# Kernel tuning notes

Measured on AMD Instinct MI355X. Metric: run time of the kernel, lower is better.

## Reference

```python
import jax, jax.numpy as jnp
import numpy as np

N, E, EMB, HID, FT, H = 2000, 32000, 768, 384, 768, 4
NEG_SLOPE = 0.2


def gat_conv(x, src, dst, edge_attr, W, a_src, a_dst, W_e, a_e, b):
    """PyG GATConv, concat=False (mean over heads), edge_dim, add_self_loops
    with fill_value='mean'. x:[N,Fin], edge_attr:[E,768]."""
    n = x.shape[0]
    h, c = a_src.shape
    # self loops: edge_attr of loop (i,i) = mean of incoming edge_attr at i
    deg = jax.ops.segment_sum(jnp.ones(src.shape[0], x.dtype), dst, num_segments=n)
    loop_attr = jax.ops.segment_sum(edge_attr, dst, num_segments=n) / jnp.maximum(deg, 1.0)[:, None]
    ar = jnp.arange(n)
    s = jnp.concatenate([src, ar])
    d = jnp.concatenate([dst, ar])
    ea = jnp.concatenate([edge_attr, loop_attr], axis=0)   # [E+N, 768]
    hx = (x @ W).reshape(n, h, c)                           # [N,H,C]
    he = (ea @ W_e).reshape(-1, h, c)                       # [E+N,H,C]
    alpha = (jnp.einsum('nhc,hc->nh', hx, a_src)[s]
             + jnp.einsum('nhc,hc->nh', hx, a_dst)[d]
             + jnp.einsum('ehc,hc->eh', he, a_e))           # [E+N,H]
    alpha = jax.nn.leaky_relu(alpha, NEG_SLOPE)
    # segment softmax over destination node (self loop guarantees nonempty)
    mx = jax.ops.segment_max(alpha, d, num_segments=n)
    ex = jnp.exp(alpha - mx[d])
    den = jax.ops.segment_sum(ex, d, num_segments=n)
    att = ex / den[d]                                       # [E+N,H]
    out = jax.ops.segment_sum(hx[s] * att[:, :, None], d, num_segments=n)  # [N,H,C]
    return out.mean(axis=1) + b


def setup_inputs() -> dict:
    key = jax.random.key(0)
    ks = jax.random.split(key, 16)
    w = lambda k, shape, s=0.05: (jax.random.normal(k, shape, jnp.float32) * s)
    return {
        'x': jax.random.randint(ks[0], (N, 2), 0, 178),
        'edge_index': jax.random.randint(ks[1], (2, E), 0, N),
        'edge_attr': jax.random.randint(ks[2], (E, 2), 0, 18),
        'x_emb': w(ks[3], (178, EMB)),
        'e_emb': w(ks[4], (18, EMB)),
        'W1': w(ks[5], (EMB, H * HID)),
        'as1': w(ks[6], (H, HID)),
        'ad1': w(ks[7], (H, HID)),
        'We1': w(ks[8], (EMB, H * HID)),
        'ae1': w(ks[9], (H, HID)),
        'b1': jnp.zeros((HID,), jnp.float32),
        'W2': w(ks[10], (HID, H * FT)),
        'as2': w(ks[11], (H, FT)),
        'ad2': w(ks[12], (H, FT)),
        'We2': w(ks[13], (EMB, H * FT)),
        'ae2': w(ks[14], (H, FT)),
        'b2': jnp.zeros((FT,), jnp.float32),
    }


def reference(x, edge_index, edge_attr, x_emb, e_emb, W1, as1, ad1, We1, ae1, b1,
              W2, as2, ad2, We2, ae2, b2):
    src, dst = edge_index[0], edge_index[1]
    xf = x_emb[x].sum(axis=1)          # [N,768]
    eaf = e_emb[edge_attr].sum(axis=1)  # [E,768]
    h = jax.nn.relu(gat_conv(xf, src, dst, eaf, W1, as1, ad1, We1, ae1, b1))
    out = gat_conv(h, src, dst, eaf, W2, as2, ad2, We2, ae2, b2)
    return out
```

## Files before the change

kernel.cpp:

```cpp
#include <hip/hip_runtime.h>
#include <hip/hip_bf16.h>

#define NN   2000
#define NE   32000
#define EMBD 768
#define NH   4
#define HID  384
#define FTD  768
#define NEG  0.2f
#define DCAP 128

#define GM 2000
#define GN 768
#define GK 1536

typedef __bf16 bf16x8 __attribute__((ext_vector_type(8)));
typedef float  f32x4  __attribute__((ext_vector_type(4)));

__device__ inline float wsum(float v){
#pragma unroll
  for (int o = 32; o > 0; o >>= 1) v += __shfl_xor(v, o, 64);
  return v;
}
__device__ inline float wmax(float v){
#pragma unroll
  for (int o = 32; o > 0; o >>= 1) v = fmaxf(v, __shfl_xor(v, o, 64));
  return v;
}

__device__ inline unsigned short f2bf(float f){
  unsigned u = __float_as_uint(f);
  unsigned r = (u + 0x7FFFu + ((u >> 16) & 1u)) >> 16;
  return (unsigned short)r;
}
__device__ inline float bf2f(unsigned short h){
  return __uint_as_float(((unsigned)h) << 16);
}

__device__ inline void gload16(const void* g, void* l){
  __builtin_amdgcn_global_load_lds((const __attribute__((address_space(1))) void*)g,
                                   (__attribute__((address_space(3))) void*)l, 16, 0, 0);
}

__global__ void k_zero(int* __restrict__ counts){
  int i = blockIdx.x * blockDim.x + threadIdx.x;
  if (i < NN) counts[i] = 0;
}

__global__ void k_count(const int* __restrict__ dst, int* __restrict__ counts){
  int e = blockIdx.x * blockDim.x + threadIdx.x;
  if (e < NE) atomicAdd(&counts[dst[e]], 1);
}

__global__ void k_scan(const int* __restrict__ counts, int* __restrict__ offsets,
                       int* __restrict__ cursor){
  __shared__ int s[1024];
  int t = threadIdx.x;
  int a = (2*t   < NN) ? counts[2*t  ] : 0;
  int b = (2*t+1 < NN) ? counts[2*t+1] : 0;
  s[t] = a + b;
  __syncthreads();
  for (int off = 1; off < 1024; off <<= 1){
    int v = (t >= off) ? s[t-off] : 0;
    __syncthreads();
    s[t] += v;
    __syncthreads();
  }
  int base = (t > 0) ? s[t-1] : 0;
  if (2*t < NN){ offsets[2*t] = base; cursor[2*t] = base; }
  if (2*t+1 < NN){ offsets[2*t+1] = base + a; cursor[2*t+1] = base + a; }
  if (2*t == NN) offsets[NN] = base;
}

__global__ void k_fill(const int* __restrict__ dst, int* __restrict__ cursor,
                       int* __restrict__ csr){
  int e = blockIdx.x * blockDim.x + threadIdx.x;
  if (e < NE){
    int p = atomicAdd(&cursor[dst[e]], 1);
    csr[p] = e;
  }
}

__global__ __launch_bounds__(256) void k_prep1(
    const float* __restrict__ We1, const float* __restrict__ ae1,
    const float* __restrict__ W2,  const float* __restrict__ as2,
    const float* __restrict__ ad2, const float* __restrict__ We2,
    const float* __restrict__ ae2,
    float* __restrict__ we_a1, float* __restrict__ wa_s2,
    float* __restrict__ wa_d2, float* __restrict__ we_a2){
  int wid = blockIdx.x*4 + (threadIdx.x >> 6);
  int lane = threadIdx.x & 63;
  if (wid < 3072){
    int k = wid >> 2, h = wid & 3;
    const float4* wr = (const float4*)(We1 + (size_t)k*1536 + h*384);
    const float4* ap = (const float4*)(ae1 + h*384);
    float4 w0 = wr[lane], a0 = ap[lane];
    float s = w0.x*a0.x + w0.y*a0.y + w0.z*a0.z + w0.w*a0.w;
    if (lane < 32){
      float4 w1 = wr[64+lane], a1 = ap[64+lane];
      s += w1.x*a1.x + w1.y*a1.y + w1.z*a1.z + w1.w*a1.w;
    }
    s = wsum(s);
    if (lane == 0) we_a1[k*4+h] = s;
  } else if (wid < 4608){
    int t2 = wid - 3072;
    int k = t2 >> 2, h = t2 & 3;
    const float4* wr = (const float4*)(W2 + (size_t)k*3072 + h*768);
    const float4* s4 = (const float4*)(as2 + h*768);
    const float4* d4 = (const float4*)(ad2 + h*768);
    float s1 = 0.f, s2 = 0.f;
#pragma unroll
    for (int i = 0; i < 3; ++i){
      float4 w = wr[i*64+lane], a = s4[i*64+lane], d = d4[i*64+lane];
      s1 += w.x*a.x + w.y*a.y + w.z*a.z + w.w*a.w;
      s2 += w.x*d.x + w.y*d.y + w.z*d.z + w.w*d.w;
    }
    s1 = wsum(s1); s2 = wsum(s2);
    if (lane == 0){ wa_s2[k*4+h] = s1; wa_d2[k*4+h] = s2; }
  } else {
    int t2 = wid - 4608;
    int k = t2 >> 2, h = t2 & 3;
    const float4* wr = (const float4*)(We2 + (size_t)k*3072 + h*768);
    const float4* ap = (const float4*)(ae2 + h*768);
    float s = 0.f;
#pragma unroll
    for (int i = 0; i < 3; ++i){
      float4 w = wr[i*64+lane], a = ap[i*64+lane];
      s += w.x*a.x + w.y*a.y + w.z*a.z + w.w*a.w;
    }
    s = wsum(s);
    if (lane == 0) we_a2[k*4+h] = s;
  }
}

__global__ __launch_bounds__(256) void k_bt(const float* __restrict__ W2,
                                            unsigned short* __restrict__ Bh,
                                            unsigned short* __restrict__ Bl){
  __shared__ float tile[64][65];
  int bk = blockIdx.x * 64;
  int bc = blockIdx.y * 64;
  int t = threadIdx.x;
  int cc = t & 63, kk4 = t >> 6;
#pragma unroll
  for (int i = 0; i < 16; ++i){
    int kk = kk4*16 + i;
    int k = bk + kk;
    int h = k / 384, kp = k - h*384;
    tile[kk][cc] = W2[(size_t)kp*3072 + h*768 + bc + cc];
  }
  __syncthreads();
  int kk2 = t & 63, cc4 = t >> 6;
#pragma unroll
  for (int i = 0; i < 16; ++i){
    int c2 = cc4*16 + i;
    float v = tile[kk2][c2];
    unsigned short hi = f2bf(v);
    unsigned short lo = f2bf(v - bf2f(hi));
    size_t o = (size_t)(bc + c2)*GK + bk + kk2;
    Bh[o] = hi; Bl[o] = lo;
  }
}

__global__ __launch_bounds__(256) void k_gemm1(const float* __restrict__ A,
                                               const float* __restrict__ B,
                                               float* __restrict__ P){
  __shared__ float As[16][34];
  __shared__ float Bs[16][68];
  int t = threadIdx.x;
  int bn = blockIdx.x * 64;
  int bm = blockIdx.y * 32;
  int s  = blockIdx.z;
  float acc[2][4] = {};
  int tm = t >> 4, tn = t & 15;
  int ar = t >> 3, ac = (t & 7) * 2;
  int br = t >> 4, bc = (t & 15) * 4;
  int kend = s*384 + 384;
  for (int k0 = s*384; k0 < kend; k0 += 16){
    float a0 = 0.f, a1 = 0.f;
    if (bm + ar < 178){
      const float* ap = &A[(size_t)(bm+ar)*EMBD + k0 + ac];
      a0 = ap[0]; a1 = ap[1];
    }
    As[ac][ar] = a0; As[ac+1][ar] = a1;
    *(float4*)&Bs[br][bc] = *(const float4*)&B[(size_t)(k0+br)*1536 + bn + bc];
    __syncthreads();
#pragma unroll
    for (int k = 0; k < 16; ++k){
      float x0 = As[k][tm*2], x1 = As[k][tm*2+1];
      float4 b4 = *(const float4*)&Bs[k][tn*4];
      acc[0][0] += x0*b4.x; acc[0][1] += x0*b4.y; acc[0][2] += x0*b4.z; acc[0][3] += x0*b4.w;
      acc[1][0] += x1*b4.x; acc[1][1] += x1*b4.y; acc[1][2] += x1*b4.z; acc[1][3] += x1*b4.w;
    }
    __syncthreads();
  }
#pragma unroll
  for (int i = 0; i < 2; ++i){
    int r = bm + tm*2 + i;
    if (r < 178){
      float4 v; v.x=acc[i][0]; v.y=acc[i][1]; v.z=acc[i][2]; v.w=acc[i][3];
      *(float4*)&P[(size_t)s*178*1536 + (size_t)r*1536 + bn + tn*4] = v;
    }
  }
}

__global__ __launch_bounds__(256) void k_prepB(
    const float* __restrict__ parts, float* __restrict__ xh1,
    const float* __restrict__ as1, const float* __restrict__ ad1,
    const float* __restrict__ e_emb,
    const float* __restrict__ we_a1, const float* __restrict__ we_a2,
    float* __restrict__ xa_s1, float* __restrict__ xa_d1,
    float* __restrict__ ew1, float* __restrict__ ew2){
  int blk = blockIdx.x, t = threadIdx.x;
  if (blk < 267){
    int i = blk*256 + t;
    float4 u = ((const float4*)parts)[i];
    float4 v = ((const float4*)parts)[68352 + i];
    float4 r; r.x=u.x+v.x; r.y=u.y+v.y; r.z=u.z+v.z; r.w=u.w+v.w;
    ((float4*)xh1)[i] = r;
  } else if (blk < 445){
    int r = blk - 267;
    int h = t >> 6, lane = t & 63;
    const float4* p0 = (const float4*)(parts + (size_t)r*1536 + h*384);
    const float4* p1 = (const float4*)(parts + (size_t)(178 + r)*1536 + h*384);
    const float4* s4 = (const float4*)(as1 + h*384);
    const float4* d4 = (const float4*)(ad1 + h*384);
    float s1, s2;
    {
      float4 a = p0[lane], b = p1[lane], sa = s4[lane], da = d4[lane];
      float4 u; u.x=a.x+b.x; u.y=a.y+b.y; u.z=a.z+b.z; u.w=a.w+b.w;
      s1 = u.x*sa.x + u.y*sa.y + u.z*sa.z + u.w*sa.w;
      s2 = u.x*da.x + u.y*da.y + u.z*da.z + u.w*da.w;
    }
    if (lane < 32){
      float4 a = p0[64+lane], b = p1[64+lane], sa = s4[64+lane], da = d4[64+lane];
      float4 u; u.x=a.x+b.x; u.y=a.y+b.y; u.z=a.z+b.z; u.w=a.w+b.w;
      s1 += u.x*sa.x + u.y*sa.y + u.z*sa.z + u.w*sa.w;
      s2 += u.x*da.x + u.y*da.y + u.z*da.z + u.w*da.w;
    }
    s1 = wsum(s1); s2 = wsum(s2);
    if (lane == 0){ xa_s1[r*4+h] = s1; xa_d1[r*4+h] = s2; }
  } else {
    int id = (blk - 445)*4 + (t >> 6);
    int lane = t & 63;
    const float* wv = (id < 72) ? we_a1 : we_a2;
    float* o = (id < 72) ? ew1 : ew2;
    int id2 = (id < 72) ? id : (id - 72);
    int r = id2 >> 2, h = id2 & 3;
    const float* ar = e_emb + (size_t)r*EMBD;
    float acc = 0.f;
    for (int k = lane; k < EMBD; k += 64) acc += ar[k] * wv[k*4+h];
    acc = wsum(acc);
    if (lane == 0) o[r*4+h] = acc;
  }
}

__global__ __launch_bounds__(384) void k_gat1(const int* __restrict__ offsets,
                      int* __restrict__ csr, const int* __restrict__ srcv,
                      const int* __restrict__ x, const int* __restrict__ ea,
                      const float* __restrict__ xa_s1, const float* __restrict__ xa_d1,
                      const float* __restrict__ ew1,
                      const float* __restrict__ xh1, const float* __restrict__ b1,
                      const float* __restrict__ wa_s2, const float* __restrict__ wa_d2,
                      float* __restrict__ spill,
                      float* __restrict__ hact,
                      float* __restrict__ asrc2, float* __restrict__ adst2){
  __shared__ float wts[DCAP][5];
  __shared__ int   sE[DCAP];
  __shared__ int   sA[DCAP], sB[DCAP];
  __shared__ float wl[4];
  __shared__ float red[6][8];
  int n = blockIdx.x, t = threadIdx.x;
  int w = t >> 6, lane = t & 63;
  int lo = offsets[n], hi = offsets[n+1];
  int deg = hi - lo;
  bool big = deg > DCAP;

  if (!big){
    int m = 1; while (m < deg) m <<= 1;
    for (int i = t; i < m; i += 384) sE[i] = (i < deg) ? csr[lo+i] : 0x7fffffff;
    __syncthreads();
    for (int k = 2; k <= m; k <<= 1){
      for (int j2 = k >> 1; j2 > 0; j2 >>= 1){
        for (int i = t; i < m; i += 384){
          int ixj = i ^ j2;
          if (ixj > i){
            int a = sE[i], b = sE[ixj];
            bool up = ((i & k) == 0);
            if ((a > b) == up){ sE[i] = b; sE[ixj] = a; }
          }
        }
        __syncthreads();
      }
    }
    for (int i = t; i < deg; i += 384) csr[lo+i] = sE[i];
  } else {
    if (t == 0){
      for (int i = lo+1; i < hi; ++i){
        int v = csr[i], j = i-1;
        while (j >= lo && csr[j] > v){ csr[j+1] = csr[j]; --j; }
        csr[j+1] = v;
      }
    }
  }
  __syncthreads();

  int xn0 = x[2*n], xn1 = x[2*n+1];
  if (w < 4){
    float ad_n = xa_d1[xn0*4+w] + xa_d1[xn1*4+w];
    float as_n = xa_s1[xn0*4+w] + xa_s1[xn1*4+w];
    float mx = -3.4e38f, sae = 0.f;
    if (!big){
      for (int j = lane; j < deg; j += 64){
        int e = sE[j]; int s = srcv[e];
        int a = x[2*s], b = x[2*s+1];
        if (w == 0){ sA[j] = a; sB[j] = b; }
        float ae = ew1[ea[2*e]*4+w] + ew1[ea[2*e+1]*4+w];
        float al = (xa_s1[a*4+w] + xa_s1[b*4+w]) + ad_n + ae;
        al = (al > 0.f) ? al : NEG * al;
        wts[j][w] = al;
        sae += ae; mx = fmaxf(mx, al);
      }
      mx = wmax(mx); sae = wsum(sae);
      float all_ = as_n + ad_n + sae / fmaxf((float)deg, 1.f);
      all_ = (all_ > 0.f) ? all_ : NEG * all_;
      mx = fmaxf(mx, all_);
      float den = 0.f;
      for (int j = lane; j < deg; j += 64){
        float xx = expf(wts[j][w] - mx);
        wts[j][w] = xx; den += xx;
      }
      den = wsum(den);
      float exl = expf(all_ - mx);
      den += exl;
      float inv = 1.f / den;
      for (int j = lane; j < deg; j += 64) wts[j][w] *= inv;
      if (lane == 0) wl[w] = exl * inv;
    } else {
      for (int p = lo + lane; p < hi; p += 64){
        int e = csr[p]; int s = srcv[e];
        int a = x[2*s], b = x[2*s+1];
        float ae = ew1[ea[2*e]*4+w] + ew1[ea[2*e+1]*4+w];
        float al = (xa_s1[a*4+w] + xa_s1[b*4+w]) + ad_n + ae;
        al = (al > 0.f) ? al : NEG * al;
        spill[e*4 + w] = al;
        sae += ae; mx = fmaxf(mx, al);
      }
      mx = wmax(mx); sae = wsum(sae);
      float all_ = as_n + ad_n + sae / fmaxf((float)deg, 1.f);
      all_ = (all_ > 0.f) ? all_ : NEG * all_;
      mx = fmaxf(mx, all_);
      float den = 0.f;
      for (int p = lo + lane; p < hi; p += 64){
        int e = csr[p];
        float xx = expf(spill[e*4 + w] - mx);
        spill[e*4 + w] = xx; den += xx;
      }
      den = wsum(den);
      float exl = expf(all_ - mx);
      den += exl;
      float inv = 1.f / den;
      for (int p = lo + lane; p < hi; p += 64) spill[csr[p]*4 + w] *= inv;
      if (lane == 0) wl[w] = exl * inv;
    }
  }
  __syncthreads();

  int c = t;
  float acc = 0.f;
  if (!big){
    float va0=0,va1=0,va2=0,va3=0,vb0=0,vb1=0,vb2=0,vb3=0;
    if (deg > 0){
      const float* pa = xh1 + (size_t)sA[0]*1536 + c;
      const float* pb = xh1 + (size_t)sB[0]*1536 + c;
      va0=pa[0]; va1=pa[384]; va2=pa[768]; va3=pa[1152];
      vb0=pb[0]; vb1=pb[384]; vb2=pb[768]; vb3=pb[1152];
    }
    for (int j = 0; j < deg; ++j){
      float ca0=va0, ca1=va1, ca2=va2, ca3=va3;
      float cb0=vb0, cb1=vb1, cb2=vb2, cb3=vb3;
      if (j+1 < deg){
        const float* pa = xh1 + (size_t)sA[j+1]*1536 + c;
        const float* pb = xh1 + (size_t)sB[j+1]*1536 + c;
        va0=pa[0]; va1=pa[384]; va2=pa[768]; va3=pa[1152];
        vb0=pb[0]; vb1=pb[384]; vb2=pb[768]; vb3=pb[1152];
      }
      float w0=wts[j][0], w1=wts[j][1], w2=wts[j][2], w3=wts[j][3];
      acc += w0*(ca0+cb0) + w1*(ca1+cb1) + w2*(ca2+cb2) + w3*(ca3+cb3);
    }
  } else {
    for (int j = 0; j < deg; ++j){
      int e = csr[lo+j]; int s = srcv[e];
      int a = x[2*s], b = x[2*s+1];
      float w0 = spill[e*4+0], w1 = spill[e*4+1], w2 = spill[e*4+2], w3 = spill[e*4+3];
      const float* pa = xh1 + (size_t)a*1536 + c;
      const float* pb = xh1 + (size_t)b*1536 + c;
      acc += w0*(pa[0]+pb[0]) + w1*(pa[384]+pb[384])
           + w2*(pa[768]+pb[768]) + w3*(pa[1152]+pb[1152]);
    }
  }
  {
    const float* pa = xh1 + (size_t)xn0*1536 + c;
    const float* pb = xh1 + (size_t)xn1*1536 + c;
    acc += wl[0]*(pa[0]+pb[0]) + wl[1]*(pa[384]+pb[384])
         + wl[2]*(pa[768]+pb[768]) + wl[3]*(pa[1152]+pb[1152]);
  }
  float v = fmaxf(0.25f*acc + b1[c], 0.f);
  hact[n*HID + c] = v;

  float pr[8];
#pragma unroll
  for (int h = 0; h < 4; ++h){ pr[h] = v * wa_s2[c*4+h]; pr[4+h] = v * wa_d2[c*4+h]; }
#pragma unroll
  for (int o = 32; o > 0; o >>= 1){
#pragma unroll
    for (int q = 0; q < 8; ++q) pr[q] += __shfl_xor(pr[q], o, 64);
  }
  if (lane == 0){
#pragma unroll
    for (int q = 0; q < 8; ++q) red[w][q] = pr[q];
  }
  __syncthreads();
  if (t < 8){
    float s2 = 0.f;
#pragma unroll
    for (int ww = 0; ww < 6; ++ww) s2 += red[ww][t];
    if (t < 4) asrc2[n*4 + t] = s2; else adst2[n*4 + t - 4] = s2;
  }
}

__global__ __launch_bounds__(384) void k_gat2(const int* __restrict__ offsets,
                      const int* __restrict__ csr, const int* __restrict__ srcv,
                      const int* __restrict__ ea,
                      const float* __restrict__ asrc, const float* __restrict__ adst,
                      const float* __restrict__ ew2,
                      const float* __restrict__ hact, float* __restrict__ spill,
                      unsigned short* __restrict__ Gh, unsigned short* __restrict__ Gl){
  __shared__ float wts[DCAP][5];
  __shared__ int   ssrc[DCAP];
  __shared__ float wl[4];
  int n = blockIdx.x, t = threadIdx.x;
  int w = t >> 6, lane = t & 63;
  int lo = offsets[n], hi = offsets[n+1];
  int deg = hi - lo;
  bool big = deg > DCAP;
  if (w < 4){
    float ad_n = adst[n*NH + w];
    float as_n = asrc[n*NH + w];
    float mx = -3.4e38f, sae = 0.f;
    if (!big){
      for (int p = lo + lane; p < hi; p += 64){
        int e = csr[p]; int s = srcv[e];
        if (w == 0) ssrc[p - lo] = s;
        float ae = ew2[ea[2*e]*4+w] + ew2[ea[2*e+1]*4+w];
        float al = asrc[s*NH + w] + ad_n + ae;
        al = (al > 0.f) ? al : NEG * al;
        wts[p - lo][w] = al;
        sae += ae; mx = fmaxf(mx, al);
      }
      mx = wmax(mx); sae = wsum(sae);
      float all_ = as_n + ad_n + sae / fmaxf((float)deg, 1.f);
      all_ = (all_ > 0.f) ? all_ : NEG * all_;
      mx = fmaxf(mx, all_);
      float den = 0.f;
      for (int p = lo + lane; p < hi; p += 64){
        float xx = expf(wts[p - lo][w] - mx);
        wts[p - lo][w] = xx; den += xx;
      }
      den = wsum(den);
      float exl = expf(all_ - mx);
      den += exl;
      float inv = 1.f / den;
      for (int p = lo + lane; p < hi; p += 64) wts[p - lo][w] *= inv;
      if (lane == 0) wl[w] = exl * inv;
    } else {
      for (int p = lo + lane; p < hi; p += 64){
        int e = csr[p];
        float ae = ew2[ea[2*e]*4+w] + ew2[ea[2*e+1]*4+w];
        float al = asrc[srcv[e]*NH + w] + ad_n + ae;
        al = (al > 0.f) ? al : NEG * al;
        spill[e*4 + w] = al;
        sae += ae; mx = fmaxf(mx, al);
      }
      mx = wmax(mx); sae = wsum(sae);
      float all_ = as_n + ad_n + sae / fmaxf((float)deg, 1.f);
      all_ = (all_ > 0.f) ? all_ : NEG * all_;
      mx = fmaxf(mx, all_);
      float den = 0.f;
      for (int p = lo + lane; p < hi; p += 64){
        int e = csr[p];
        float xx = expf(spill[e*4 + w] - mx);
        spill[e*4 + w] = xx; den += xx;
      }
      den = wsum(den);
      float exl = expf(all_ - mx);
      den += exl;
      float inv = 1.f / den;
      for (int p = lo + lane; p < hi; p += 64) spill[csr[p]*4 + w] *= inv;
      if (lane == 0) wl[w] = exl * inv;
    }
  }
  __syncthreads();

  int c = t;
  float a0 = 0.f, a1 = 0.f, a2 = 0.f, a3 = 0.f;
  if (!big){
    float vnext = 0.f;
    if (deg > 0) vnext = hact[(size_t)ssrc[0]*HID + c];
    for (int j = 0; j < deg; ++j){
      float vc = vnext;
      if (j+1 < deg) vnext = hact[(size_t)ssrc[j+1]*HID + c];
      float w0=wts[j][0], w1=wts[j][1], w2=wts[j][2], w3=wts[j][3];
      a0 += w0*vc; a1 += w1*vc; a2 += w2*vc; a3 += w3*vc;
    }
  } else {
    for (int j = 0; j < deg; ++j){
      int e = csr[lo+j]; int s = srcv[e];
      float w0 = spill[e*4+0], w1 = spill[e*4+1], w2 = spill[e*4+2], w3 = spill[e*4+3];
      float vc = hact[(size_t)s*HID + c];
      a0 += w0*vc; a1 += w1*vc; a2 += w2*vc; a3 += w3*vc;
    }
  }
  {
    float vc = hact[(size_t)n*HID + c];
    a0 += wl[0]*vc; a1 += wl[1]*vc; a2 += wl[2]*vc; a3 += wl[3]*vc;
  }
  size_t base = (size_t)n*GK + c;
  float vv[4] = {a0, a1, a2, a3};
#pragma unroll
  for (int h = 0; h < 4; ++h){
    unsigned short hi16 = f2bf(vv[h]);
    unsigned short lo16 = f2bf(vv[h] - bf2f(hi16));
    Gh[base + h*384] = hi16;
    Gl[base + h*384] = lo16;
  }
}

__global__ __launch_bounds__(256) void k_mm2(const unsigned short* __restrict__ Gh,
                                             const unsigned short* __restrict__ Gl,
                                             const unsigned short* __restrict__ Bh,
                                             const unsigned short* __restrict__ Bl,
                                             const float* __restrict__ b2,
                                             float* __restrict__ out){
  __shared__ __align__(16) unsigned short lds[2][4][64][64];
  int b = blockIdx.x;
  int xcd = b & 7, idx = b >> 3;
  int bm = xcd*4 + idx/12, bn = idx % 12;
  int wave = threadIdx.x >> 6, lane = threadIdx.x & 63;
  int wm = wave >> 1, wn = wave & 1;
  int rl = lane & 15, kq = lane >> 4;

  int rt   = lane >> 3;
  int kswz = ((lane & 7) ^ rt) * 8;
  const unsigned short* sbase;
  int rowbase;
  if (wave == 0){ sbase = Gh; rowbase = bm*64; }
  else if (wave == 1){ sbase = Gl; rowbase = bm*64; }
  else if (wave == 2){ sbase = Bh; rowbase = bn*64; }
  else { sbase = Bl; rowbase = bn*64; }
  bool isA = wave < 2;

  f32x4 acc[2][2] = {};

#pragma unroll
  for (int i = 0; i < 8; ++i){
    int row = rowbase + i*8 + rt;
    if (isA) row = (row < GM) ? row : (GM-1);
    gload16(sbase + (size_t)row*GK + kswz, &lds[0][wave][i*8][0]);
  }
  __syncthreads();

  for (int t = 0; t < 24; ++t){
    int cur = t & 1;
    if (t < 23){
      int k0 = (t+1)*64;
#pragma unroll
      for (int i = 0; i < 8; ++i){
        int row = rowbase + i*8 + rt;
        if (isA) row = (row < GM) ? row : (GM-1);
        gload16(sbase + (size_t)row*GK + k0 + kswz, &lds[cur^1][wave][i*8][0]);
      }
    }
#pragma unroll
    for (int ks = 0; ks < 2; ++ks){
      bf16x8 ah[2], al2[2], bh2[2], bl2[2];
#pragma unroll
      for (int i = 0; i < 2; ++i){
        int r = wm*32 + i*16 + rl;
        int sl = (ks*4 + kq) ^ (r & 7);
        ah[i]  = *(const bf16x8*)&lds[cur][0][r][sl*8];
        al2[i] = *(const bf16x8*)&lds[cur][1][r][sl*8];
      }
#pragma unroll
      for (int j = 0; j < 2; ++j){
        int cdx = wn*32 + j*16 + rl;
        int sl = (ks*4 + kq) ^ (cdx & 7);
        bh2[j] = *(const bf16x8*)&lds[cur][2][cdx][sl*8];
        bl2[j] = *(const bf16x8*)&lds[cur][3][cdx][sl*8];
      }
#pragma unroll
      for (int i = 0; i < 2; ++i){
#pragma unroll
        for (int j = 0; j < 2; ++j){
          acc[i][j] = __builtin_amdgcn_mfma_f32_16x16x32_bf16(ah[i],  bh2[j], acc[i][j], 0, 0, 0);
          acc[i][j] = __builtin_amdgcn_mfma_f32_16x16x32_bf16(ah[i],  bl2[j], acc[i][j], 0, 0, 0);
          acc[i][j] = __builtin_amdgcn_mfma_f32_16x16x32_bf16(al2[i], bh2[j], acc[i][j], 0, 0, 0);
        }
      }
    }
    __syncthreads();
  }

#pragma unroll
  for (int i = 0; i < 2; ++i){
#pragma unroll
    for (int j = 0; j < 2; ++j){
      int col = bn*64 + wn*32 + j*16 + rl;
      float bb = b2[col];
#pragma unroll
      for (int r = 0; r < 4; ++r){
        int row = bm*64 + wm*32 + i*16 + kq*4 + r;
        if (row < GM) out[(size_t)row*GN + col] = 0.25f*acc[i][j][r] + bb;
      }
    }
  }
}

extern "C" void kernel_launch(void* const* d_in, const int* in_sizes, int n_in,
                              void* d_out, int out_size, void* d_ws, size_t ws_size,
                              hipStream_t stream){
  const int*   x     = (const int*)d_in[0];
  const int*   ei    = (const int*)d_in[1];
  const int*   ea    = (const int*)d_in[2];
  const float* x_emb = (const float*)d_in[3];
  const float* e_emb = (const float*)d_in[4];
  const float* W1    = (const float*)d_in[5];
  const float* as1   = (const float*)d_in[6];
  const float* ad1   = (const float*)d_in[7];
  const float* We1   = (const float*)d_in[8];
  const float* ae1   = (const float*)d_in[9];
  const float* b1    = (const float*)d_in[10];
  const float* W2    = (const float*)d_in[11];
  const float* as2   = (const float*)d_in[12];
  const float* ad2   = (const float*)d_in[13];
  const float* We2   = (const float*)d_in[14];
  const float* ae2   = (const float*)d_in[15];
  const float* b2    = (const float*)d_in[16];
  const int* srcv = ei;
  const int* dstv = ei + NE;
  float* out = (float*)d_out;

  char* p = (char*)d_ws;
  auto take = [&](size_t n){ void* q = (void*)p; p += (n + 255) & ~(size_t)255; return q; };
  int*   counts  = (int*)take(NN*4);
  int*   cursor  = (int*)take(NN*4);
  int*   offsets = (int*)take((NN+1)*4);
  int*   csr     = (int*)take(NE*4);
  float* we_a1   = (float*)take(EMBD*NH*4);
  float* wa_s2   = (float*)take(HID*NH*4);
  float* wa_d2   = (float*)take(HID*NH*4);
  float* we_a2   = (float*)take(EMBD*NH*4);
  float* xa_s1   = (float*)take(178*NH*4);
  float* xa_d1   = (float*)take(178*NH*4);
  float* ew1     = (float*)take(18*NH*4);
  float* ew2     = (float*)take(18*NH*4);
  float* xh1     = (float*)take((size_t)178*1536*4);
  float* parts1  = (float*)take((size_t)2*178*1536*4);
  unsigned short* Bth = (unsigned short*)take((size_t)GN*GK*2);
  unsigned short* Btl = (unsigned short*)take((size_t)GN*GK*2);
  unsigned short* Gh  = (unsigned short*)take((size_t)GM*GK*2);
  unsigned short* Gl  = (unsigned short*)take((size_t)GM*GK*2);
  float* spill   = (float*)take((size_t)NE*NH*4);
  float* hact    = (float*)take((size_t)NN*HID*4);
  float* asrc2   = (float*)take(NN*NH*4);
  float* adst2   = (float*)take(NN*NH*4);

  k_zero<<<8, 256, 0, stream>>>(counts);
  k_count<<<(NE+255)/256, 256, 0, stream>>>(dstv, counts);
  k_scan<<<1, 1024, 0, stream>>>(counts, offsets, cursor);
  k_fill<<<(NE+255)/256, 256, 0, stream>>>(dstv, cursor, csr);

  k_prep1<<<1920, 256, 0, stream>>>(We1, ae1, W2, as2, ad2, We2, ae2,
                                    we_a1, wa_s2, wa_d2, we_a2);
  { dim3 g(GK/64, GN/64); k_bt<<<g, 256, 0, stream>>>(W2, Bth, Btl); }
  { dim3 g(24, 6, 2); k_gemm1<<<g, 256, 0, stream>>>(x_emb, W1, parts1); }
  k_prepB<<<481, 256, 0, stream>>>(parts1, xh1, as1, ad1, e_emb, we_a1, we_a2,
                                   xa_s1, xa_d1, ew1, ew2);

  k_gat1<<<NN, 384, 0, stream>>>(offsets, csr, srcv, x, ea, xa_s1, xa_d1, ew1,
                                 xh1, b1, wa_s2, wa_d2, spill, hact, asrc2, adst2);

  k_gat2<<<NN, 384, 0, stream>>>(offsets, csr, srcv, ea, asrc2, adst2, ew2,
                                 hact, spill, Gh, Gl);

  k_mm2<<<384, 256, 0, stream>>>(Gh, Gl, Bth, Btl, b2, out);
}
```

Baseline: 132.0 us.

## Reformulate layer-1 aggregation as per-token coefficient matrix times bf16x3 MFMA GEMM

Layer-1 aggregation is rewritten to exploit the fact that node features come from only 178 embedding tokens. Each node accumulates attention weights per (head, token) into a 768-wide coefficient row, split into bf16 hi/lo parts. A new MFMA GEMM then multiplies this matrix by a transposed, padded per-token projection table to produce the hidden activations. This replaces per-edge gathers of 1536-float rows with a dense GEMM; the attention-score dot products move into a separate small kernel. The serial lane-0 scatter into shared memory and the extra launches add cost in exchange.

```diff
diff --git a/kernel.cpp b/kernel.cpp
--- a/kernel.cpp
+++ b/kernel.cpp
@@ -6,13 +6,13 @@
 #define EMBD 768
 #define NH   4
 #define HID  384
-#define FTD  768
 #define NEG  0.2f
 #define DCAP 128
 
 #define GM 2000
 #define GN 768
 #define GK 1536
+#define K1 768
 
 typedef __bf16 bf16x8 __attribute__((ext_vector_type(8)));
 typedef float  f32x4  __attribute__((ext_vector_type(4)));
@@ -204,21 +204,25 @@
 }
 
 __global__ __launch_bounds__(256) void k_prepB(
-    const float* __restrict__ parts, float* __restrict__ xh1,
+    const float* __restrict__ parts,
     const float* __restrict__ as1, const float* __restrict__ ad1,
     const float* __restrict__ e_emb,
     const float* __restrict__ we_a1, const float* __restrict__ we_a2,
+    unsigned short* __restrict__ XHh, unsigned short* __restrict__ XHl,
     float* __restrict__ xa_s1, float* __restrict__ xa_d1,
     float* __restrict__ ew1, float* __restrict__ ew2){
   int blk = blockIdx.x, t = threadIdx.x;
-  if (blk < 267){
-    int i = blk*256 + t;
-    float4 u = ((const float4*)parts)[i];
-    float4 v = ((const float4*)parts)[68352 + i];
-    float4 r; r.x=u.x+v.x; r.y=u.y+v.y; r.z=u.z+v.z; r.w=u.w+v.w;
-    ((float4*)xh1)[i] = r;
-  } else if (blk < 445){
-    int r = blk - 267;
+  if (blk < 178){
+    int tok = blk;
+    for (int i = t; i < 1536; i += 256){
+      float v = parts[(size_t)tok*1536 + i] + parts[(size_t)(178+tok)*1536 + i];
+      int h = i / 384, c = i - h*384;
+      size_t off = (size_t)c*K1 + h*192 + tok;
+      unsigned short hi = f2bf(v);
+      XHh[off] = hi; XHl[off] = f2bf(v - bf2f(hi));
+    }
+  } else if (blk < 356){
+    int r = blk - 178;
     int h = t >> 6, lane = t & 63;
     const float4* p0 = (const float4*)(parts + (size_t)r*1536 + h*384);
     const float4* p1 = (const float4*)(parts + (size_t)(178 + r)*1536 + h*384);
@@ -239,8 +243,8 @@
     }
     s1 = wsum(s1); s2 = wsum(s2);
     if (lane == 0){ xa_s1[r*4+h] = s1; xa_d1[r*4+h] = s2; }
-  } else {
-    int id = (blk - 445)*4 + (t >> 6);
+  } else if (blk < 392){
+    int id = (blk - 356)*4 + (t >> 6);
     int lane = t & 63;
     const float* wv = (id < 72) ? we_a1 : we_a2;
     float* o = (id < 72) ? ew1 : ew2;
@@ -251,24 +255,27 @@
     for (int k = lane; k < EMBD; k += 64) acc += ar[k] * wv[k*4+h];
     acc = wsum(acc);
     if (lane == 0) o[r*4+h] = acc;
-  }
-}
-
-__global__ __launch_bounds__(384) void k_gat1(const int* __restrict__ offsets,
+  } else {
+    int i = (blk - 392)*256 + t;
+    if (i < 21504){
+      int c = i / 56, rem = i - c*56;
+      int h = rem / 14, tp = 178 + rem - h*14;
+      size_t off = (size_t)c*K1 + h*192 + tp;
+      XHh[off] = 0; XHl[off] = 0;
+    }
+  }
+}
+
+__global__ __launch_bounds__(256) void k_gat1sm(const int* __restrict__ offsets,
                       int* __restrict__ csr, const int* __restrict__ srcv,
                       const int* __restrict__ x, const int* __restrict__ ea,
                       const float* __restrict__ xa_s1, const float* __restrict__ xa_d1,
-                      const float* __restrict__ ew1,
-                      const float* __restrict__ xh1, const float* __restrict__ b1,
-                      const float* __restrict__ wa_s2, const float* __restrict__ wa_d2,
-                      float* __restrict__ spill,
-                      float* __restrict__ hact,
-                      float* __restrict__ asrc2, float* __restrict__ adst2){
+                      const float* __restrict__ ew1, float* __restrict__ spill,
+                      unsigned short* __restrict__ Qh, unsigned short* __restrict__ Ql){
   __shared__ float wts[DCAP][5];
   __shared__ int   sE[DCAP];
   __shared__ int   sA[DCAP], sB[DCAP];
-  __shared__ float wl[4];
-  __shared__ float red[6][8];
+  __shared__ float coef[K1];
   int n = blockIdx.x, t = threadIdx.x;
   int w = t >> 6, lane = t & 63;
   int lo = offsets[n], hi = offsets[n+1];
@@ -277,11 +284,11 @@
 
   if (!big){
     int m = 1; while (m < deg) m <<= 1;
-    for (int i = t; i < m; i += 384) sE[i] = (i < deg) ? csr[lo+i] : 0x7fffffff;
+    for (int i = t; i < m; i += 256) sE[i] = (i < deg) ? csr[lo+i] : 0x7fffffff;
     __syncthreads();
     for (int k = 2; k <= m; k <<= 1){
       for (int j2 = k >> 1; j2 > 0; j2 >>= 1){
-        for (int i = t; i < m; i += 384){
+        for (int i = t; i < m; i += 256){
           int ixj = i ^ j2;
           if (ixj > i){
             int a = sE[i], b = sE[ixj];
@@ -292,7 +299,7 @@
         __syncthreads();
       }
     }
-    for (int i = t; i < deg; i += 384) csr[lo+i] = sE[i];
+    for (int i = t; i < deg; i += 256) csr[lo+i] = sE[i];
   } else {
     if (t == 0){
       for (int i = lo+1; i < hi; ++i){
@@ -302,114 +309,201 @@
       }
     }
   }
+  for (int i = t; i < K1; i += 256) coef[i] = 0.f;
   __syncthreads();
 
   int xn0 = x[2*n], xn1 = x[2*n+1];
-  if (w < 4){
-    float ad_n = xa_d1[xn0*4+w] + xa_d1[xn1*4+w];
-    float as_n = xa_s1[xn0*4+w] + xa_s1[xn1*4+w];
-    float mx = -3.4e38f, sae = 0.f;
+  float ad_n = xa_d1[xn0*4+w] + xa_d1[xn1*4+w];
+  float as_n = xa_s1[xn0*4+w] + xa_s1[xn1*4+w];
+  float mx = -3.4e38f, sae = 0.f;
+  float wlv;
+  if (!big){
+    for (int j = lane; j < deg; j += 64){
+      int e = sE[j]; int s = srcv[e];
+      int a = x[2*s], b = x[2*s+1];
+      if (w == 0){ sA[j] = a; sB[j] = b; }
+      float ae = ew1[ea[2*e]*4+w] + ew1[ea[2*e+1]*4+w];
+      float al = (xa_s1[a*4+w] + xa_s1[b*4+w]) + ad_n + ae;
+      al = (al > 0.f) ? al : NEG * al;
+      wts[j][w] = al;
+      sae += ae; mx = fmaxf(mx, al);
+    }
+    mx = wmax(mx); sae = wsum(sae);
+    float all_ = as_n + ad_n + sae / fmaxf((float)deg, 1.f);
+    all_ = (all_ > 0.f) ? all_ : NEG * all_;
+    mx = fmaxf(mx, all_);
+    float den = 0.f;
+    for (int j = lane; j < deg; j += 64){
+      float xx = expf(wts[j][w] - mx);
+      wts[j][w] = xx; den += xx;
+    }
+    den = wsum(den);
+    float exl = expf(all_ - mx);
+    den += exl;
+    float inv = 1.f / den;
+    for (int j = lane; j < deg; j += 64) wts[j][w] *= inv;
+    wlv = exl * inv;
+  } else {
+    for (int p = lo + lane; p < hi; p += 64){
+      int e = csr[p]; int s = srcv[e];
+      int a = x[2*s], b = x[2*s+1];
+      float ae = ew1[ea[2*e]*4+w] + ew1[ea[2*e+1]*4+w];
+      float al = (xa_s1[a*4+w] + xa_s1[b*4+w]) + ad_n + ae;
+      al = (al > 0.f) ? al : NEG * al;
+      spill[e*4 + w] = al;
+      sae += ae; mx = fmaxf(mx, al);
+    }
+    mx = wmax(mx); sae = wsum(sae);
+    float all_ = as_n + ad_n + sae / fmaxf((float)deg, 1.f);
+    all_ = (all_ > 0.f) ? all_ : NEG * all_;
+    mx = fmaxf(mx, all_);
+    float den = 0.f;
+    for (int p = lo + lane; p < hi; p += 64){
+      int e = csr[p];
+      float xx = expf(spill[e*4 + w] - mx);
+      spill[e*4 + w] = xx; den += xx;
+    }
+    den = wsum(den);
+    float exl = expf(all_ - mx);
+    den += exl;
+    float inv = 1.f / den;
+    for (int p = lo + lane; p < hi; p += 64) spill[csr[p]*4 + w] *= inv;
+    wlv = exl * inv;
+  }
+  __syncthreads();
+
+  if (lane == 0){
+    float* cf = coef + w*192;
     if (!big){
-      for (int j = lane; j < deg; j += 64){
-        int e = sE[j]; int s = srcv[e];
-        int a = x[2*s], b = x[2*s+1];
-        if (w == 0){ sA[j] = a; sB[j] = b; }
-        float ae = ew1[ea[2*e]*4+w] + ew1[ea[2*e+1]*4+w];
-        float al = (xa_s1[a*4+w] + xa_s1[b*4+w]) + ad_n + ae;
-        al = (al > 0.f) ? al : NEG * al;
-        wts[j][w] = al;
-        sae += ae; mx = fmaxf(mx, al);
-      }
-      mx = wmax(mx); sae = wsum(sae);
-      float all_ = as_n + ad_n + sae / fmaxf((float)deg, 1.f);
-      all_ = (all_ > 0.f) ? all_ : NEG * all_;
-      mx = fmaxf(mx, all_);
-      float den = 0.f;
-      for (int j = lane; j < deg; j += 64){
-        float xx = expf(wts[j][w] - mx);
-        wts[j][w] = xx; den += xx;
-      }
-      den = wsum(den);
-      float exl = expf(all_ - mx);
-      den += exl;
-      float inv = 1.f / den;
-      for (int j = lane; j < deg; j += 64) wts[j][w] *= inv;
-      if (lane == 0) wl[w] = exl * inv;
+      for (int j = 0; j < deg; ++j){
+        float wj = wts[j][w];
+        cf[sA[j]] += wj; cf[sB[j]] += wj;
+      }
     } else {
-      for (int p = lo + lane; p < hi; p += 64){
+      for (int p = lo; p < hi; ++p){
         int e = csr[p]; int s = srcv[e];
-        int a = x[2*s], b = x[2*s+1];
-        float ae = ew1[ea[2*e]*4+w] + ew1[ea[2*e+1]*4+w];
-        float al = (xa_s1[a*4+w] + xa_s1[b*4+w]) + ad_n + ae;
-        al = (al > 0.f) ? al : NEG * al;
-        spill[e*4 + w] = al;
-        sae += ae; mx = fmaxf(mx, al);
-      }
-      mx = wmax(mx); sae = wsum(sae);
-      float all_ = as_n + ad_n + sae / fmaxf((float)deg, 1.f);
-      all_ = (all_ > 0.f) ? all_ : NEG * all_;
-      mx = fmaxf(mx, all_);
-      float den = 0.f;
-      for (int p = lo + lane; p < hi; p += 64){
-        int e = csr[p];
-        float xx = expf(spill[e*4 + w] - mx);
-        spill[e*4 + w] = xx; den += xx;
-      }
-      den = wsum(den);
-      float exl = expf(all_ - mx);
-      den += exl;
-      float inv = 1.f / den;
-      for (int p = lo + lane; p < hi; p += 64) spill[csr[p]*4 + w] *= inv;
-      if (lane == 0) wl[w] = exl * inv;
-    }
+        float wj = spill[e*4 + w];
+        cf[x[2*s]] += wj; cf[x[2*s+1]] += wj;
+      }
+    }
+    cf[xn0] += wlv; cf[xn1] += wlv;
   }
   __syncthreads();
 
-  int c = t;
-  float acc = 0.f;
-  if (!big){
-    float va0=0,va1=0,va2=0,va3=0,vb0=0,vb1=0,vb2=0,vb3=0;
-    if (deg > 0){
-      const float* pa = xh1 + (size_t)sA[0]*1536 + c;
-      const float* pb = xh1 + (size_t)sB[0]*1536 + c;
-      va0=pa[0]; va1=pa[384]; va2=pa[768]; va3=pa[1152];
-      vb0=pb[0]; vb1=pb[384]; vb2=pb[768]; vb3=pb[1152];
-    }
-    for (int j = 0; j < deg; ++j){
-      float ca0=va0, ca1=va1, ca2=va2, ca3=va3;
-      float cb0=vb0, cb1=vb1, cb2=vb2, cb3=vb3;
-      if (j+1 < deg){
-        const float* pa = xh1 + (size_t)sA[j+1]*1536 + c;
-        const float* pb = xh1 + (size_t)sB[j+1]*1536 + c;
-        va0=pa[0]; va1=pa[384]; va2=pa[768]; va3=pa[1152];
-        vb0=pb[0]; vb1=pb[384]; vb2=pb[768]; vb3=pb[1152];
-      }
-      float w0=wts[j][0], w1=wts[j][1], w2=wts[j][2], w3=wts[j][3];
-      acc += w0*(ca0+cb0) + w1*(ca1+cb1) + w2*(ca2+cb2) + w3*(ca3+cb3);
-    }
-  } else {
-    for (int j = 0; j < deg; ++j){
-      int e = csr[lo+j]; int s = srcv[e];
-      int a = x[2*s], b = x[2*s+1];
-      float w0 = spill[e*4+0], w1 = spill[e*4+1], w2 = spill[e*4+2], w3 = spill[e*4+3];
-      const float* pa = xh1 + (size_t)a*1536 + c;
-      const float* pb = xh1 + (size_t)b*1536 + c;
-      acc += w0*(pa[0]+pb[0]) + w1*(pa[384]+pb[384])
-           + w2*(pa[768]+pb[768]) + w3*(pa[1152]+pb[1152]);
-    }
-  }
-  {
-    const float* pa = xh1 + (size_t)xn0*1536 + c;
-    const float* pb = xh1 + (size_t)xn1*1536 + c;
-    acc += wl[0]*(pa[0]+pb[0]) + wl[1]*(pa[384]+pb[384])
-         + wl[2]*(pa[768]+pb[768]) + wl[3]*(pa[1152]+pb[1152]);
-  }
-  float v = fmaxf(0.25f*acc + b1[c], 0.f);
-  hact[n*HID + c] = v;
-
-  float pr[8];
-#pragma unroll
-  for (int h = 0; h < 4; ++h){ pr[h] = v * wa_s2[c*4+h]; pr[4+h] = v * wa_d2[c*4+h]; }
+  for (int i = t; i < K1; i += 256){
+    float v = coef[i];
+    unsigned short hi16 = f2bf(v);
+    Qh[(size_t)n*K1 + i] = hi16;
+    Ql[(size_t)n*K1 + i] = f2bf(v - bf2f(hi16));
+  }
+}
+
+__global__ __launch_bounds__(256) void k_mm1(const unsigned short* __restrict__ Qh,
+                                             const unsigned short* __restrict__ Ql,
+                                             const unsigned short* __restrict__ XHh,
+                                             const unsigned short* __restrict__ XHl,
+                                             const float* __restrict__ b1,
+                                             float* __restrict__ hact){
+  __shared__ __align__(16) unsigned short lds[2][4][64][64];
+  int b = blockIdx.x;
+  int xcd = b & 7, idx = b >> 3;
+  int bm = xcd*4 + idx/6, bn = idx % 6;
+  int wave = threadIdx.x >> 6, lane = threadIdx.x & 63;
+  int wm = wave >> 1, wn = wave & 1;
+  int rl = lane & 15, kq = lane >> 4;
+
+  int rt   = lane >> 3;
+  int kswz = ((lane & 7) ^ rt) * 8;
+  const unsigned short* sbase;
+  int rowbase;
+  if (wave == 0){ sbase = Qh; rowbase = bm*64; }
+  else if (wave == 1){ sbase = Ql; rowbase = bm*64; }
+  else if (wave == 2){ sbase = XHh; rowbase = bn*64; }
+  else { sbase = XHl; rowbase = bn*64; }
+  bool isA = wave < 2;
+
+  f32x4 acc[2][2] = {};
+
+#pragma unroll
+  for (int i = 0; i < 8; ++i){
+    int row = rowbase + i*8 + rt;
+    if (isA) row = (row < GM) ? row : (GM-1);
+    gload16(sbase + (size_t)row*K1 + kswz, &lds[0][wave][i*8][0]);
+  }
+  __syncthreads();
+
+  for (int t = 0; t < 12; ++t){
+    int cur = t & 1;
+    if (t < 11){
+      int k0 = (t+1)*64;
+#pragma unroll
+      for (int i = 0; i < 8; ++i){
+        int row = rowbase + i*8 + rt;
+        if (isA) row = (row < GM) ? row : (GM-1);
+        gload16(sbase + (size_t)row*K1 + k0 + kswz, &lds[cur^1][wave][i*8][0]);
+      }
+    }
+#pragma unroll
+    for (int ks = 0; ks < 2; ++ks){
+      bf16x8 ah[2], al2[2], bh2[2], bl2[2];
+#pragma unroll
+      for (int i = 0; i < 2; ++i){
+        int r = wm*32 + i*16 + rl;
+        int sl = (ks*4 + kq) ^ (r & 7);
+        ah[i]  = *(const bf16x8*)&lds[cur][0][r][sl*8];
+        al2[i] = *(const bf16x8*)&lds[cur][1][r][sl*8];
+      }
+#pragma unroll
+      for (int j = 0; j < 2; ++j){
+        int cdx = wn*32 + j*16 + rl;
+        int sl = (ks*4 + kq) ^ (cdx & 7);
+        bh2[j] = *(const bf16x8*)&lds[cur][2][cdx][sl*8];
+        bl2[j] = *(const bf16x8*)&lds[cur][3][cdx][sl*8];
+      }
+#pragma unroll
+      for (int i = 0; i < 2; ++i){
+#pragma unroll
+        for (int j = 0; j < 2; ++j){
+          acc[i][j] = __builtin_amdgcn_mfma_f32_16x16x32_bf16(ah[i],  bh2[j], acc[i][j], 0, 0, 0);
+          acc[i][j] = __builtin_amdgcn_mfma_f32_16x16x32_bf16(ah[i],  bl2[j], acc[i][j], 0, 0, 0);
+          acc[i][j] = __builtin_amdgcn_mfma_f32_16x16x32_bf16(al2[i], bh2[j], acc[i][j], 0, 0, 0);
+        }
+      }
+    }
+    __syncthreads();
+  }
+
+#pragma unroll
+  for (int i = 0; i < 2; ++i){
+#pragma unroll
+    for (int j = 0; j < 2; ++j){
+      int col = bn*64 + wn*32 + j*16 + rl;
+      float bb = b1[col];
+#pragma unroll
+      for (int r = 0; r < 4; ++r){
+        int row = bm*64 + wm*32 + i*16 + kq*4 + r;
+        if (row < GM) hact[(size_t)row*HID + col] = fmaxf(0.25f*acc[i][j][r] + bb, 0.f);
+      }
+    }
+  }
+}
+
+__global__ __launch_bounds__(256) void k_dots(const float* __restrict__ hact,
+                      const float* __restrict__ wa_s2, const float* __restrict__ wa_d2,
+                      float* __restrict__ asrc2, float* __restrict__ adst2){
+  int w = threadIdx.x >> 6, lane = threadIdx.x & 63;
+  int n = blockIdx.x*4 + w;
+  float pr[8] = {};
+#pragma unroll
+  for (int i = 0; i < 6; ++i){
+    int c = i*64 + lane;
+    float v = hact[(size_t)n*HID + c];
+#pragma unroll
+    for (int h = 0; h < 4; ++h){
+      pr[h]   += v * wa_s2[c*4+h];
+      pr[4+h] += v * wa_d2[c*4+h];
+    }
+  }
 #pragma unroll
   for (int o = 32; o > 0; o >>= 1){
 #pragma unroll
@@ -417,14 +511,7 @@
   }
   if (lane == 0){
 #pragma unroll
-    for (int q = 0; q < 8; ++q) red[w][q] = pr[q];
-  }
-  __syncthreads();
-  if (t < 8){
-    float s2 = 0.f;
-#pragma unroll
-    for (int ww = 0; ww < 6; ++ww) s2 += red[ww][t];
-    if (t < 4) asrc2[n*4 + t] = s2; else adst2[n*4 + t - 4] = s2;
+    for (int h = 0; h < 4; ++h){ asrc2[n*4+h] = pr[h]; adst2[n*4+h] = pr[4+h]; }
   }
 }
 
@@ -663,8 +750,11 @@
   float* xa_d1   = (float*)take(178*NH*4);
   float* ew1     = (float*)take(18*NH*4);
   float* ew2     = (float*)take(18*NH*4);
-  float* xh1     = (float*)take((size_t)178*1536*4);
   float* parts1  = (float*)take((size_t)2*178*1536*4);
+  unsigned short* XHh = (unsigned short*)take((size_t)HID*K1*2);
+  unsigned short* XHl = (unsigned short*)take((size_t)HID*K1*2);
+  unsigned short* Qh  = (unsigned short*)take((size_t)NN*K1*2);
+  unsigned short* Ql  = (unsigned short*)take((size_t)NN*K1*2);
   unsigned short* Bth = (unsigned short*)take((size_t)GN*GK*2);
   unsigned short* Btl = (unsigned short*)take((size_t)GN*GK*2);
   unsigned short* Gh  = (unsigned short*)take((size_t)GM*GK*2);
@@ -683,11 +773,13 @@
                                     we_a1, wa_s2, wa_d2, we_a2);
   { dim3 g(GK/64, GN/64); k_bt<<<g, 256, 0, stream>>>(W2, Bth, Btl); }
   { dim3 g(24, 6, 2); k_gemm1<<<g, 256, 0, stream>>>(x_emb, W1, parts1); }
-  k_prepB<<<481, 256, 0, stream>>>(parts1, xh1, as1, ad1, e_emb, we_a1, we_a2,
-                                   xa_s1, xa_d1, ew1, ew2);
-
-  k_gat1<<<NN, 384, 0, stream>>>(offsets, csr, srcv, x, ea, xa_s1, xa_d1, ew1,
-                                 xh1, b1, wa_s2, wa_d2, spill, hact, asrc2, adst2);
+  k_prepB<<<476, 256, 0, stream>>>(parts1, as1, ad1, e_emb, we_a1, we_a2,
+                                   XHh, XHl, xa_s1, xa_d1, ew1, ew2);
+
+  k_gat1sm<<<NN, 256, 0, stream>>>(offsets, csr, srcv, x, ea, xa_s1, xa_d1,
+                                   ew1, spill, Qh, Ql);
+  k_mm1<<<192, 256, 0, stream>>>(Qh, Ql, XHh, XHl, b1, hact);
+  k_dots<<<500, 256, 0, stream>>>(hact, wa_s2, wa_d2, asrc2, adst2);
 
   k_gat2<<<NN, 384, 0, stream>>>(offsets, csr, srcv, ea, asrc2, adst2, ew2,
                                  hact, spill, Gh, Gl);
```

Result: no change. 131.7 us (-0.2%).
